# Kernel optimization log

Hardware: AMD Instinct MI355X
Metric: run time of the kernel (lower is better)

Reference implementation:

```python
import jax, jax.numpy as jnp
import numpy as np

A = 3                      # anchors per location
HS = [256, 128, 64, 32]    # square feature-map sizes (FPN levels)
B = 4                      # batch (num images)
SIZES = [A * h * h for h in HS]
T = sum(SIZES)             # 261120 anchors per image
PRE_N, POST_N = 512, 512
NMS_TH, SCORE_TH, MIN_SIZE = 0.7, 0.0, 1e-3
LOG_MAX = 4.135166556742356   # log(1000/16), standard delta clamp
MAXV = 8                      # max vertices of quad-quad intersection
LVL_OFF = 8192.0              # per-level coordinate offset for batched NMS


def box_corners(b):
    # b: [..., 5] (cx, cy, w, h, angle) -> [..., 4, 2] CCW corners
    cx, cy, w, h, a = (b[..., i] for i in range(5))
    c, s = jnp.cos(a), jnp.sin(a)
    dx = 0.5 * jnp.stack([w, -w, -w, w], -1)
    dy = 0.5 * jnp.stack([h, h, -h, -h], -1)
    x = cx[..., None] + dx * c[..., None] - dy * s[..., None]
    y = cy[..., None] + dx * s[..., None] + dy * c[..., None]
    return jnp.stack([x, y], -1)


def _clip(poly, cnt, p1, p2):
    # Sutherland-Hodgman clip of poly (padded [MAXV,2], cnt valid) by half-plane left of p1->p2
    e = p2 - p1
    d = e[0] * (poly[:, 1] - p1[1]) - e[1] * (poly[:, 0] - p1[0])
    def body(carry, i):
        out, oc = carry
        nxt = jnp.where(i + 1 < cnt, i + 1, 0)
        cur_in, nxt_in = d[i] >= 0, d[nxt] >= 0
        valid = i < cnt
        keep = valid & cur_in
        out = out.at[oc].set(jnp.where(keep, poly[i], out[oc]))
        oc = oc + keep.astype(jnp.int32)
        crs = valid & (cur_in != nxt_in)
        den = d[i] - d[nxt]
        t = d[i] / jnp.where(den == 0, 1.0, den)
        ip = poly[i] + t * (poly[nxt] - poly[i])
        out = out.at[oc].set(jnp.where(crs, ip, out[oc]))
        oc = oc + crs.astype(jnp.int32)
        return (out, oc), None
    (out, oc), _ = jax.lax.scan(body, (jnp.zeros((MAXV, 2), poly.dtype), jnp.int32(0)), jnp.arange(MAXV))
    return out, oc


def _inter_area(ca, cb):
    # intersection area of two convex quads given CCW corners [4,2]
    poly = jnp.zeros((MAXV, 2), ca.dtype).at[:4].set(ca)
    cnt = jnp.int32(4)
    for k in range(4):
        poly, cnt = _clip(poly, cnt, cb[k], cb[(k + 1) % 4])
    i = jnp.arange(MAXV)
    nxt = jnp.where(i + 1 < cnt, i + 1, 0)
    cr = poly[i, 0] * poly[nxt, 1] - poly[nxt, 0] * poly[i, 1]
    area = 0.5 * jnp.abs(jnp.sum(jnp.where(i < cnt, cr, 0.0)))
    return jnp.where(cnt >= 3, area, 0.0)


def decode(deltas, anchors):
    # XYWHA decode with 6-dim deltas (dx,dy,dw,dh,dsin,dcos), weights all 1.0
    ax, ay, aw, ah, aa = (anchors[..., i] for i in range(5))
    dx, dy, dw, dh, ds, dc = (deltas[..., i] for i in range(6))
    dw = jnp.minimum(dw, LOG_MAX)
    dh = jnp.minimum(dh, LOG_MAX)
    return jnp.stack([ax + dx * aw, ay + dy * ah, aw * jnp.exp(dw),
                      ah * jnp.exp(dh), aa + jnp.arctan2(ds, dc)], -1)


def nms_image(boxes, scores, levels):
    # boxes [N,5], scores [N] (post-sigmoid), levels [N] int32 -> fixed-size padded outputs
    N = scores.shape[0]
    valid = (boxes[:, 2] >= MIN_SIZE) & (boxes[:, 3] >= MIN_SIZE) & (scores >= SCORE_TH)
    s = jnp.where(valid, scores, -jnp.inf)
    order = jnp.argsort(-s)
    bx, sc, vd = boxes[order], s[order], valid[order]
    off = levels[order].astype(bx.dtype) * LVL_OFF
    nb = bx.at[:, :2].add(off[:, None])          # level offset => cross-level IoU == 0
    nbg = jax.lax.stop_gradient(nb)
    corners = box_corners(nbg)                    # [N,4,2]
    areas = nbg[:, 2] * nbg[:, 3]
    CH = 128
    def chunk_fn(args):
        cc, ca = args
        def row(ci, ai):
            inter = jax.vmap(lambda cj: _inter_area(ci, cj))(corners)
            return inter / (ai + areas - inter + 1e-7)
        return jax.vmap(row)(cc, ca)
    iou = jax.lax.map(chunk_fn, (corners.reshape(N // CH, CH, 4, 2),
                                 areas.reshape(N // CH, CH))).reshape(N, N)
    idx = jnp.arange(N)
    def body(i, sup):
        keep_i = ~sup[i]
        return sup | (keep_i & (iou[i] > NMS_TH) & (idx > i))
    sup = jax.lax.fori_loop(0, N, body, ~vd)      # invalid boxes start suppressed
    kept = ~sup
    _, top_i = jax.lax.top_k(jnp.where(kept, sc, -jnp.inf), POST_N)
    ok = kept[top_i]
    return jnp.where(ok[:, None], bx[top_i], 0.0), jnp.where(ok, sc[top_i], 0.0)


def rpn_forward(objs, dlts, anchors):
    obj_f, dlt_f = [], []
    for o, d, h in zip(objs, dlts, HS):
        # permute_and_flatten: [B,A,H,W] -> [B,H*W*A]; [B,A*6,H,W] -> [B,H*W*A,6]
        obj_f.append(o.transpose(0, 2, 3, 1).reshape(B, -1))
        dlt_f.append(d.reshape(B, A, 6, h, h).transpose(0, 3, 4, 1, 2).reshape(B, -1, 6))
    objectness = jnp.concatenate(obj_f, 1)        # [B, T]
    deltas = jnp.concatenate(dlt_f, 1)            # [B, T, 6]
    proposals = decode(deltas, anchors)           # [B, T, 5]
    parts, offset = [], 0
    for sz in SIZES:                               # per-level top-k
        k = min(PRE_N, sz)
        _, ti = jax.lax.top_k(objectness[:, offset:offset + sz], k)
        parts.append(ti + offset)
        offset += sz
    top_idx = jnp.concatenate(parts, 1)           # [B, 4*PRE_N]
    levels = jnp.concatenate([jnp.full((sz,), i, jnp.int32) for i, sz in enumerate(SIZES)])
    obj_top = jnp.take_along_axis(objectness, top_idx, 1)
    prop_top = jnp.take_along_axis(proposals, top_idx[..., None], 1)
    lvl_top = levels[top_idx]
    scores = jax.nn.sigmoid(obj_top)
    return jax.vmap(nms_image)(prop_top, scores, lvl_top)


def setup_inputs() -> dict:
    key = jax.random.key(0)
    ks = jax.random.split(key, 9)
    inp = {}
    for i, h in enumerate(HS):
        inp[f"obj{i}"] = jax.random.normal(ks[i], (B, A, h, h), jnp.float32)
        inp[f"dlt{i}"] = 0.25 * jax.random.normal(ks[4 + i], (B, A * 6, h, h), jnp.float32)
    u = jax.random.uniform(ks[8], (B, T, 5), jnp.float32)
    inp["anchors"] = jnp.stack([u[..., 0] * 1024.0, u[..., 1] * 1024.0,
                                8.0 + 120.0 * u[..., 2], 8.0 + 120.0 * u[..., 3],
                                jnp.pi * (u[..., 4] - 0.5)], -1)
    return inp


def reference(obj0, obj1, obj2, obj3, dlt0, dlt1, dlt2, dlt3, anchors):
    # returns (boxes [B, POST_N, 5], scores [B, POST_N]) padded with zeros
    return rpn_forward([obj0, obj1, obj2, obj3], [dlt0, dlt1, dlt2, dlt3], anchors)
```

## Files before the change

kernel.cpp:

```cpp
#include <hip/hip_runtime.h>

typedef unsigned int u32;
typedef unsigned long long u64;
typedef unsigned char u8;

#define NB 4
#define T_ANCH 261120
#define NCAND 2048
#define KSEL 512
#define POSTN 512
#define LOG_MAXF 4.135166556742356f
#define NMS_TH 0.7f
#define LVL_OFF_F 8192.0f
#define BINS 4096
#define EQCAP 8192
#define PAIR_CAP (1u<<20)
#define K4A_BLOCKS 2048
#define K4A_ROWS 4
#define K1_BLOCKS 256

__device__ __forceinline__ u32 mono32(float f){
  u32 u = __float_as_uint(f);
  return (u & 0x80000000u) ? ~u : (u | 0x80000000u);
}
__device__ __forceinline__ int lvl_hw(int lvl){ return 65536 >> (2*lvl); }
__device__ __forceinline__ int lvl_off(int lvl){
  return (lvl>0?196608:0) + (lvl>1?49152:0) + (lvl>2?12288:0);
}
__device__ __forceinline__ void k1_map(int bx, int& b, int& lvl, int& ch){
  b = bx >> 6;
  int c = bx & 63;
  if (c < 48){ lvl = 0; ch = c; }
  else if (c < 60){ lvl = 1; ch = c - 48; }
  else if (c < 63){ lvl = 2; ch = c - 60; }
  else { lvl = 3; ch = 0; }
}

__global__ __launch_bounds__(1024) void k1a_hist(
    const float* __restrict__ o0, const float* __restrict__ o1,
    const float* __restrict__ o2, const float* __restrict__ o3,
    u32* __restrict__ ghist)
{
  int b, lvl, ch;
  k1_map(blockIdx.x, b, lvl, ch);
  const float* ob = (lvl==0)?o0 : (lvl==1)?o1 : (lvl==2)?o2 : o3;
  int hw = lvl_hw(lvl);
  int size = 3*hw;
  int n4 = size >> 2;
  int i4 = ch*1024 + threadIdx.x;
  __shared__ u32 hist[BINS];
  for (int i = threadIdx.x; i < BINS; i += 1024) hist[i] = 0;
  __syncthreads();
  if (i4 < n4){
    float4 v = ((const float4*)(ob + (size_t)b*size))[i4];
    atomicAdd(&hist[mono32(v.x) >> 20], 1u);
    atomicAdd(&hist[mono32(v.y) >> 20], 1u);
    atomicAdd(&hist[mono32(v.z) >> 20], 1u);
    atomicAdd(&hist[mono32(v.w) >> 20], 1u);
  }
  __syncthreads();
  u32* out = ghist + (size_t)blockIdx.x*BINS;
  for (int i = threadIdx.x; i < BINS; i += 1024) out[i] = hist[i];
}

__global__ __launch_bounds__(1024) void k1b_thresh(
    const u32* __restrict__ ghist, u32* __restrict__ gb0,
    u32* __restrict__ gcA, u32* __restrict__ emitcnt, u32* __restrict__ tiecnt)
{
  int bid = blockIdx.x;
  int b = bid >> 2, lvl = bid & 3;
  int base_bx = b*64 + (lvl==0?0 : lvl==1?48 : lvl==2?60 : 63);
  int nch = (lvl==0?48 : lvl==1?12 : lvl==2?3 : 1);
  __shared__ u32 hist[BINS];
  __shared__ u32 coarse[64];
  int t = threadIdx.x;
  u32 c0=0,c1=0,c2=0,c3=0;
  for (int ch = 0; ch < nch; ++ch){
    const u32* h = ghist + (size_t)(base_bx+ch)*BINS;
    c0 += h[4*t+0]; c1 += h[4*t+1]; c2 += h[4*t+2]; c3 += h[4*t+3];
  }
  hist[4*t+0]=c0; hist[4*t+1]=c1; hist[4*t+2]=c2; hist[4*t+3]=c3;
  __syncthreads();
  if (t < 64){
    u32 s = 0;
    for (int z = 0; z < 64; ++z) s += hist[t*64 + z];
    coarse[t] = s;
  }
  __syncthreads();
  if (t == 0){
    u32 acc = 0;
    int cb = 63;
    while (acc + coarse[cb] < (u32)KSEL){ acc += coarse[cb]; --cb; }
    int z = cb*64 + 63;
    while (acc + hist[z] < (u32)KSEL){ acc += hist[z]; --z; }
    gb0[bid] = (u32)z;
    gcA[bid] = acc;
    emitcnt[bid] = 0;
    tiecnt[bid] = 0;
  }
}

__global__ __launch_bounds__(1024) void k1c_classify(
    const float* __restrict__ o0, const float* __restrict__ o1,
    const float* __restrict__ o2, const float* __restrict__ o3,
    const u32* __restrict__ gb0,
    u32* __restrict__ emitcnt, u32* __restrict__ tiecnt,
    int* __restrict__ cand_j, u64* __restrict__ gtie)
{
  int b, lvl, ch;
  k1_map(blockIdx.x, b, lvl, ch);
  int bid16 = b*4 + lvl;
  const float* ob = (lvl==0)?o0 : (lvl==1)?o1 : (lvl==2)?o2 : o3;
  int hw = lvl_hw(lvl);
  int size = 3*hw;
  int n4 = size >> 2;
  int i4 = ch*1024 + threadIdx.x;

  __shared__ u32 dbuf[KSEL];
  __shared__ u64 tbuf[4096];
  __shared__ u32 dn, tn, dbase, tbase;
  if (threadIdx.x == 0){ dn = 0; tn = 0; }
  __syncthreads();

  u32 b0v = gb0[bid16];
  if (i4 < n4){
    float4 v = ((const float4*)(ob + (size_t)b*size))[i4];
    int L = i4 << 2;
    int a = L / hw;
    int pix = L - a*hw;
    int j0 = pix*3 + a;
    float vv[4] = {v.x, v.y, v.z, v.w};
    #pragma unroll
    for (int q = 0; q < 4; ++q){
      u32 m = mono32(vv[q]);
      u32 bin = m >> 20;
      int j = j0 + 3*q;
      if (bin > b0v){
        u32 s = atomicAdd(&dn, 1u);
        if (s < (u32)KSEL) dbuf[s] = (u32)j;
      } else if (bin == b0v){
        u32 s = atomicAdd(&tn, 1u);
        if (s < 4096u) tbuf[s] = ((u64)m << 32) | (u32)(~(u32)j);
      }
    }
  }
  __syncthreads();
  if (threadIdx.x == 0){
    dbase = dn ? atomicAdd(&emitcnt[bid16], dn) : 0u;
    tbase = tn ? atomicAdd(&tiecnt[bid16], tn) : 0u;
  }
  __syncthreads();
  for (u32 x = threadIdx.x; x < dn; x += 1024){
    u32 s = dbase + x;
    if (s < (u32)KSEL) cand_j[bid16*KSEL + s] = (int)dbuf[x];
  }
  for (u32 x = threadIdx.x; x < tn; x += 1024){
    u32 s = tbase + x;
    if (s < (u32)EQCAP) gtie[(size_t)bid16*EQCAP + s] = tbuf[x];
  }
}

__global__ __launch_bounds__(1024) void k1d_tie(
    const u64* __restrict__ gtie, const u32* __restrict__ tiecnt,
    const u32* __restrict__ gcA, u32* __restrict__ emitcnt,
    int* __restrict__ cand_j)
{
  int bid = blockIdx.x;
  __shared__ u64 eq[EQCAP];
  __shared__ u32 wbuf[KSEL];
  __shared__ u32 wn, wbase;
  u32 n = tiecnt[bid]; if (n > (u32)EQCAP) n = (u32)EQCAP;
  u32 k = (u32)KSEL - gcA[bid];
  if (threadIdx.x == 0) wn = 0;
  for (u32 i = threadIdx.x; i < n; i += 1024) eq[i] = gtie[(size_t)bid*EQCAP + i];
  __syncthreads();
  for (u32 i = threadIdx.x; i < n; i += 1024){
    u64 ki = eq[i];
    u32 r = 0;
    for (u32 m = 0; m < n; ++m) r += (eq[m] > ki) ? 1u : 0u;
    if (r < k){
      u32 s = atomicAdd(&wn, 1u);
      if (s < (u32)KSEL) wbuf[s] = (u32)(~(u32)ki);
    }
  }
  __syncthreads();
  if (threadIdx.x == 0) wbase = wn ? atomicAdd(&emitcnt[bid], wn) : 0u;
  __syncthreads();
  for (u32 x = threadIdx.x; x < wn; x += 1024){
    u32 s = wbase + x;
    if (s < (u32)KSEL) cand_j[bid*KSEL + s] = (int)wbuf[x];
  }
}

__global__ __launch_bounds__(256) void k2_decode(
    const float* __restrict__ o0, const float* __restrict__ o1,
    const float* __restrict__ o2, const float* __restrict__ o3,
    const float* __restrict__ d0, const float* __restrict__ d1,
    const float* __restrict__ d2, const float* __restrict__ d3,
    const float* __restrict__ anchors,
    const int* __restrict__ cand_j,
    float* __restrict__ cscore, u32* __restrict__ csmono,
    u64* __restrict__ ctb, float* __restrict__ cbox, u8* __restrict__ cvalid)
{
  int c = blockIdx.x*256 + threadIdx.x;
  if (c >= NB*NCAND) return;
  int pair = c >> 9;
  int b = pair >> 2, lvl = pair & 3;
  int j = cand_j[c];
  int hw = lvl_hw(lvl);
  u32 pix = (u32)j / 3u;
  u32 a = (u32)j - pix*3u;
  const float* ob = (lvl==0)?o0 : (lvl==1)?o1 : (lvl==2)?o2 : o3;
  const float* dl = (lvl==0)?d0 : (lvl==1)?d1 : (lvl==2)?d2 : d3;

  float ov = ob[(size_t)(b*3 + (int)a)*hw + pix];
  size_t dbase = ((size_t)(b*3 + (int)a)*6)*(size_t)hw + pix;
  float dx  = dl[dbase + 0*(size_t)hw];
  float dy  = dl[dbase + 1*(size_t)hw];
  float dw  = dl[dbase + 2*(size_t)hw];
  float dh  = dl[dbase + 3*(size_t)hw];
  float dsn = dl[dbase + 4*(size_t)hw];
  float dcs = dl[dbase + 5*(size_t)hw];
  int tt = lvl_off(lvl) + j;
  const float* an = anchors + ((size_t)b*T_ANCH + tt)*5;
  float ax=an[0], ay=an[1], aw=an[2], ah=an[3], aa=an[4];
  dw = fminf(dw, LOG_MAXF); dh = fminf(dh, LOG_MAXF);
  float cx = ax + dx*aw;
  float cy = ay + dy*ah;
  float w  = aw * expf(dw);
  float h  = ah * expf(dh);
  float ang = aa + atan2f(dsn, dcs);
  double sd = 1.0 / (1.0 + exp(-(double)ov));
  float sc = (float)sd;
  bool valid = (w >= 1e-3f) && (h >= 1e-3f) && (sc >= 0.0f);
  cscore[c] = sc;
  csmono[c] = valid ? mono32(sc) : 0u;
  ctb[c] = ((u64)lvl << 50) | ((u64)(u32)(~mono32(ov)) << 18) | (u64)(u32)j;
  cvalid[c] = valid ? 1 : 0;
  float* bb = cbox + (size_t)c*5;
  bb[0]=cx; bb[1]=cy; bb[2]=w; bb[3]=h; bb[4]=ang;
}

__global__ __launch_bounds__(256) void k3_rank(
    const u32* __restrict__ csmono, const u64* __restrict__ ctb,
    const float* __restrict__ cscore, const float* __restrict__ cbox,
    const u8* __restrict__ cvalid,
    float* __restrict__ sscore, float* __restrict__ sbox,
    float* __restrict__ geom, float4* __restrict__ aabb4,
    u8* __restrict__ svalid)
{
  int b   = blockIdx.x >> 6;
  int blk = blockIdx.x & 63;
  __shared__ u32 sm[NCAND];
  __shared__ u64 stb[NCAND];
  __shared__ u32 cnt[32][8];
  for (int k = threadIdx.x; k < NCAND; k += 256){
    sm[k]  = csmono[b*NCAND + k];
    stb[k] = ctb[b*NCAND + k];
  }
  __syncthreads();
  int esub = threadIdx.x >> 3;
  int ssub = threadIdx.x & 7;
  int id = blk*32 + esub;
  u32 ms = sm[id];
  u64 mt = stb[id];
  u32 r = 0;
  #pragma unroll 8
  for (int it = 0; it < 256; ++it){
    int m = it*8 + ssub;
    u32 s2 = sm[m]; u64 t2 = stb[m];
    r += ((s2 > ms) || (s2 == ms && t2 < mt)) ? 1u : 0u;
  }
  cnt[esub][ssub] = r;
  __syncthreads();
  if (ssub == 0){
    u32 rank = 0;
    #pragma unroll
    for (int q = 0; q < 8; ++q) rank += cnt[esub][q];
    int gsrc = b*NCAND + id;
    int gdst = b*NCAND + (int)rank;
    sscore[gdst] = cscore[gsrc];
    svalid[gdst] = cvalid[gsrc];
    float b0 = cbox[(size_t)gsrc*5+0], b1 = cbox[(size_t)gsrc*5+1];
    float b2 = cbox[(size_t)gsrc*5+2], b3 = cbox[(size_t)gsrc*5+3];
    float b4 = cbox[(size_t)gsrc*5+4];
    float* sb = sbox + (size_t)gdst*5;
    sb[0]=b0; sb[1]=b1; sb[2]=b2; sb[3]=b3; sb[4]=b4;
    int lvl = (int)((mt >> 50) & 3ull);
    float offv = (float)lvl * LVL_OFF_F;
    float cx = b0 + offv, cy = b1 + offv, w=b2, h=b3, ang=b4;
    float cc = cosf(ang), sn = sinf(ang);
    float hx = 0.5f*w, hy = 0.5f*h;
    float x0 = cx + hx*cc - hy*sn, y0 = cy + hx*sn + hy*cc;
    float x1 = cx - hx*cc - hy*sn, y1 = cy - hx*sn + hy*cc;
    float x2 = cx - hx*cc + hy*sn, y2 = cy - hx*sn - hy*cc;
    float x3 = cx + hx*cc + hy*sn, y3 = cy + hx*sn - hy*cc;
    float minx = fminf(fminf(x0,x1),fminf(x2,x3));
    float maxx = fmaxf(fmaxf(x0,x1),fmaxf(x2,x3));
    float miny = fminf(fminf(y0,y1),fminf(y2,y3));
    float maxy = fmaxf(fmaxf(y0,y1),fmaxf(y2,y3));
    float* g = geom + (size_t)gdst*16;
    g[0]=minx; g[1]=maxx; g[2]=miny; g[3]=maxy; g[4]=w*h;
    g[5]=x0; g[6]=y0; g[7]=x1; g[8]=y1; g[9]=x2; g[10]=y2; g[11]=x3; g[12]=y3;
    aabb4[gdst] = make_float4(minx, maxx, miny, maxy);
  }
}

__global__ __launch_bounds__(256) void k4a_aabb(
    const float4* __restrict__ aabb4,
    u32* __restrict__ list, u32* __restrict__ gcount)
{
  __shared__ u32 lbuf[K4A_ROWS*NCAND];
  __shared__ u32 lcnt, lbase;
  if (threadIdx.x == 0) lcnt = 0;
  __syncthreads();
  int img = blockIdx.x >> 9;
  int i0  = (blockIdx.x & 511) * K4A_ROWS;
  #pragma unroll
  for (int r = 0; r < K4A_ROWS; ++r){
    int i = i0 + r;
    float4 gi = aabb4[img*NCAND + i];
    for (int j = threadIdx.x; j < NCAND; j += 256){
      bool pass = false;
      if (j > i){
        float4 gj = aabb4[img*NCAND + j];
        pass = !(gi.x > gj.y || gj.x > gi.y || gi.z > gj.w || gj.z > gi.w);
      }
      if (pass){
        u32 s = atomicAdd(&lcnt, 1u);
        lbuf[s] = (u32)((img << 22) | (i << 11) | j);
      }
    }
  }
  __syncthreads();
  if (threadIdx.x == 0) lbase = lcnt ? atomicAdd(gcount, lcnt) : 0u;
  __syncthreads();
  u32 n = lcnt, bs = lbase;
  for (u32 x = threadIdx.x; x < n; x += 256){
    u32 idx = bs + x;
    if (idx < PAIR_CAP) list[idx] = lbuf[x];
  }
}

__device__ __forceinline__ void emit_pt(float* ox, float* oy, int oc, float x, float y){
  #pragma unroll
  for (int s = 0; s < 8; ++s) if (s == oc){ ox[s] = x; oy[s] = y; }
}

__device__ float quad_inter(const float* ca, const float* cb){
  float px[8], py[8];
  #pragma unroll
  for (int q = 0; q < 8; ++q){ px[q]=0.f; py[q]=0.f; }
  #pragma unroll
  for (int q = 0; q < 4; ++q){ px[q]=ca[2*q]; py[q]=ca[2*q+1]; }
  int cnt = 4;
  #pragma unroll
  for (int e = 0; e < 4; ++e){
    float p1x = cb[2*e],         p1y = cb[2*e+1];
    float p2x = cb[(2*e+2)&7],   p2y = cb[(2*e+3)&7];
    float ex = p2x-p1x, ey = p2y-p1y;
    float d[8];
    #pragma unroll
    for (int q = 0; q < 8; ++q) d[q] = ex*(py[q]-p1y) - ey*(px[q]-p1x);
    float ox[8], oy[8];
    #pragma unroll
    for (int q = 0; q < 8; ++q){ ox[q]=0.f; oy[q]=0.f; }
    int oc = 0;
    #pragma unroll
    for (int q = 0; q < 8; ++q){
      if (q < cnt){
        bool last = (q+1 >= cnt);
        float dn  = last ? d[0]  : d[(q+1)&7];
        bool in0 = (d[q] >= 0.0f), in1 = (dn >= 0.0f);
        if (in0){ emit_pt(ox,oy,oc,px[q],py[q]); oc++; }
        if (in0 != in1){
          float pnx = last ? px[0] : px[(q+1)&7];
          float pny = last ? py[0] : py[(q+1)&7];
          float den = d[q] - dn;
          float t = d[q] / ((den == 0.0f) ? 1.0f : den);
          emit_pt(ox,oy,oc, px[q] + t*(pnx-px[q]), py[q] + t*(pny-py[q]));
          oc++;
        }
      }
    }
    cnt = (oc > 8) ? 8 : oc;
    #pragma unroll
    for (int q = 0; q < 8; ++q){ px[q]=ox[q]; py[q]=oy[q]; }
  }
  if (cnt < 3) return 0.0f;
  float s = 0.0f;
  #pragma unroll
  for (int q = 0; q < 8; ++q){
    if (q < cnt){
      bool last = (q+1 >= cnt);
      float pnx = last ? px[0] : px[(q+1)&7];
      float pny = last ? py[0] : py[(q+1)&7];
      s += px[q]*pny - pnx*py[q];
    }
  }
  return 0.5f*fabsf(s);
}

__global__ __launch_bounds__(256) void k4b_clip(
    const float* __restrict__ geom, const u32* __restrict__ list,
    const u32* __restrict__ gcount, u64* __restrict__ mask,
    u64* __restrict__ rowflag)
{
  u32 count = *gcount;
  if (count > PAIR_CAP) count = PAIR_CAP;
  for (u32 idx = blockIdx.x*256 + threadIdx.x; idx < count; idx += gridDim.x*256){
    u32 gt = list[idx];
    int img = (int)(gt >> 22);
    int rem = (int)(gt & ((1u<<22)-1));
    int i = rem >> 11;
    int j = rem & (NCAND-1);
    const float* gi = geom + ((size_t)(img*NCAND + i))*16;
    const float* gj = geom + ((size_t)(img*NCAND + j))*16;
    float inter = quad_inter(gi+5, gj+5);
    float iou = inter / (gi[4] + gj[4] - inter + 1e-7f);
    if (iou > NMS_TH){
      atomicOr(&mask[((size_t)(img*NCAND + i))*32 + (j >> 6)], 1ull << (j & 63));
      atomicOr(&rowflag[(size_t)img*32 + (i >> 6)], 1ull << (i & 63));
    }
  }
}

__global__ __launch_bounds__(1024) void k5_nms_out(
    const u64* __restrict__ mask, const u64* __restrict__ rowflag,
    const u8* __restrict__ svalid,
    const float* __restrict__ sbox, const float* __restrict__ sscore,
    float* __restrict__ out)
{
  int b = blockIdx.x;
  __shared__ u32 fid[NCAND];
  __shared__ u32 wcnt[32], wpref[32];
  __shared__ u64 s_kept[32];
  __shared__ u32 pref[32];
  __shared__ u32 s_F;
  int t = threadIdx.x;
  int wid = t >> 6, lane = t & 63;

  if (t < 32) wcnt[t] = (u32)__popcll(rowflag[b*32 + t]);
  __syncthreads();
  if (t == 0){
    u32 run = 0;
    for (int w = 0; w < 32; ++w){ wpref[w] = run; run += wcnt[w]; }
    s_F = run;
  }
  __syncthreads();
  if (t < 32){
    u64 fw = rowflag[b*32 + t];
    u32 o = wpref[t];
    while (fw){
      int bpos = __builtin_ctzll(fw);
      fid[o++] = (u32)(t*64 + bpos);
      fw &= fw - 1;
    }
  }
  for (int x = t; x < POSTN*5; x += 1024) out[(size_t)b*POSTN*5 + x] = 0.0f;
  for (int x = t; x < POSTN;   x += 1024) out[(size_t)NB*POSTN*5 + b*POSTN + x] = 0.0f;
  __syncthreads();

  if (wid == 0){
    u32 slo = 0, shi = 0;
    {
      int wl = lane & 31;
      u64 w = 0;
      for (int q = 0; q < 64; ++q)
        if (!svalid[b*NCAND + wl*64 + q]) w |= (1ull << q);
      slo = (u32)w; shi = (u32)(w >> 32);
    }
    u32 F = s_F;
    const u64* mb = mask + ((size_t)b*NCAND)*32;
    for (u32 f = 0; f < F; f += 8){
      u32 myfid = 0;
      if (f + (lane & 7) < F) myfid = fid[f + (lane & 7)];
      u64 v[8];
      #pragma unroll
      for (int q = 0; q < 8; ++q){
        if (f + q < F){
          u32 fq = (u32)__builtin_amdgcn_readlane((int)myfid, q);
          v[q] = mb[(size_t)fq*32 + (lane & 31)];
        } else v[q] = 0ull;
      }
      #pragma unroll
      for (int q = 0; q < 8; ++q){
        if (f + q < F){
          u32 i = (u32)__builtin_amdgcn_readlane((int)myfid, q);
          int wi = (int)(i >> 6);
          u32 wlo = (u32)__builtin_amdgcn_readlane((int)slo, wi);
          u32 whi = (u32)__builtin_amdgcn_readlane((int)shi, wi);
          u64 w = ((u64)whi << 32) | wlo;
          u32 keep = (u32)((~w >> (i & 63)) & 1ull);
          u64 vm = v[q] & (0ull - (u64)keep);
          slo |= (u32)vm; shi |= (u32)(vm >> 32);
        }
      }
    }
    if (lane < 32) s_kept[lane] = ~(((u64)shi << 32) | slo);
  }
  __syncthreads();

  if (t < 32) pref[t] = (u32)__popcll(s_kept[t]);
  __syncthreads();
  if (t == 0){
    u32 run = 0;
    for (int w = 0; w < 32; ++w){ u32 tv = pref[w]; pref[w] = run; run += tv; }
  }
  __syncthreads();
  for (int i = t; i < NCAND; i += 1024){
    u64 kw = s_kept[i >> 6];
    if ((kw >> (i & 63)) & 1ull){
      u32 rank = pref[i >> 6] + (u32)__popcll(kw & ((1ull << (i & 63)) - 1ull));
      if (rank < POSTN){
        const float* bp = sbox + ((size_t)(b*NCAND + i))*5;
        float* op = out + ((size_t)(b*POSTN + rank))*5;
        op[0]=bp[0]; op[1]=bp[1]; op[2]=bp[2]; op[3]=bp[3]; op[4]=bp[4];
        out[(size_t)NB*POSTN*5 + b*POSTN + rank] = sscore[b*NCAND + i];
      }
    }
  }
}

extern "C" void kernel_launch(void* const* d_in, const int* in_sizes, int n_in,
                              void* d_out, int out_size, void* d_ws, size_t ws_size,
                              hipStream_t stream)
{
  (void)out_size; (void)ws_size;
  const float *obj[4] = {nullptr,nullptr,nullptr,nullptr};
  const float *dlt[4] = {nullptr,nullptr,nullptr,nullptr};
  const float *anchors = nullptr;
  for (int i = 0; i < n_in; ++i){
    int s = in_sizes[i];
    const float* p = (const float*)d_in[i];
    switch (s){
      case 786432:  obj[0] = p; break;
      case 4718592: dlt[0] = p; break;
      case 196608:  obj[1] = p; break;
      case 1179648: dlt[1] = p; break;
      case 49152:   obj[2] = p; break;
      case 294912:  dlt[2] = p; break;
      case 12288:   obj[3] = p; break;
      case 73728:   dlt[3] = p; break;
      case 5222400: anchors = p; break;
      default: break;
    }
  }

  char* wsb = (char*)d_ws;
  size_t off = 0;
  auto alloc = [&](size_t bytes)->void*{
    size_t cur = (off + 255) & ~(size_t)255;
    off = cur + bytes;
    return (void*)(wsb + cur);
  };
  int*   cand_j = (int*)  alloc(16*KSEL*sizeof(int));
  float* cscore = (float*)alloc((size_t)NB*NCAND*sizeof(float));
  u32*   csmono = (u32*)  alloc((size_t)NB*NCAND*sizeof(u32));
  u64*   ctb    = (u64*)  alloc((size_t)NB*NCAND*sizeof(u64));
  float* cbox   = (float*)alloc((size_t)NB*NCAND*5*sizeof(float));
  u8*    cvalid = (u8*)   alloc((size_t)NB*NCAND);
  float* sscore = (float*)alloc((size_t)NB*NCAND*sizeof(float));
  float* sbox   = (float*)alloc((size_t)NB*NCAND*5*sizeof(float));
  u8*    svalid = (u8*)   alloc((size_t)NB*NCAND);
  float* geom   = (float*)alloc((size_t)NB*NCAND*16*sizeof(float));
  float4* aabb4 = (float4*)alloc((size_t)NB*NCAND*sizeof(float4));
  size_t mask_bytes = (size_t)NB*NCAND*32*sizeof(u64);
  u64*   maskp  = (u64*)  alloc(mask_bytes);
  u64*   rowflag= (u64*)  alloc((size_t)NB*32*sizeof(u64));
  u32*   pcount = (u32*)  alloc(sizeof(u32));
  u32*   plist  = (u32*)  alloc((size_t)PAIR_CAP*sizeof(u32));
  u32*   ghist  = (u32*)  alloc((size_t)K1_BLOCKS*BINS*sizeof(u32));
  u64*   gtie   = (u64*)  alloc((size_t)16*EQCAP*sizeof(u64));
  u32*   gb0    = (u32*)  alloc(16*sizeof(u32));
  u32*   gcA    = (u32*)  alloc(16*sizeof(u32));
  u32*   emitc  = (u32*)  alloc(16*sizeof(u32));
  u32*   tiec   = (u32*)  alloc(16*sizeof(u32));

  hipMemsetAsync(maskp, 0, mask_bytes + (size_t)NB*32*sizeof(u64) + 256, stream);

  hipLaunchKernelGGL(k1a_hist, dim3(K1_BLOCKS), dim3(1024), 0, stream,
                     obj[0], obj[1], obj[2], obj[3], ghist);
  hipLaunchKernelGGL(k1b_thresh, dim3(16), dim3(1024), 0, stream,
                     ghist, gb0, gcA, emitc, tiec);
  hipLaunchKernelGGL(k1c_classify, dim3(K1_BLOCKS), dim3(1024), 0, stream,
                     obj[0], obj[1], obj[2], obj[3], gb0, emitc, tiec,
                     cand_j, gtie);
  hipLaunchKernelGGL(k1d_tie, dim3(16), dim3(1024), 0, stream,
                     gtie, tiec, gcA, emitc, cand_j);
  hipLaunchKernelGGL(k2_decode, dim3(32), dim3(256), 0, stream,
                     obj[0], obj[1], obj[2], obj[3],
                     dlt[0], dlt[1], dlt[2], dlt[3],
                     anchors, cand_j, cscore, csmono, ctb, cbox, cvalid);
  hipLaunchKernelGGL(k3_rank, dim3(256), dim3(256), 0, stream,
                     csmono, ctb, cscore, cbox, cvalid, sscore, sbox, geom,
                     aabb4, svalid);
  hipLaunchKernelGGL(k4a_aabb, dim3(K4A_BLOCKS), dim3(256), 0, stream,
                     aabb4, plist, pcount);
  hipLaunchKernelGGL(k4b_clip, dim3(256), dim3(256), 0, stream,
                     geom, plist, pcount, maskp, rowflag);
  hipLaunchKernelGGL(k5_nms_out, dim3(4), dim3(1024), 0, stream,
                     maskp, rowflag, svalid, sbox, sscore, (float*)d_out);
}
```

Baseline: 200.5 us.

## Fuse pipeline stages to cut kernel launches and global round-trips

Merges the histogram and threshold kernels using global atomic histograms and a last-block-done counter, so the final block per (image, level) computes the threshold. Tie resolution is fused with box decode, and the AABB pair filter is fused with the quad clipping, which removes the global pair list. The aim is to cut launch count and intermediate global traffic. In exchange, clipping load is now spread unevenly across blocks, and extra atomics and fences are added.

```diff
diff --git a/kernel.cpp b/kernel.cpp
--- a/kernel.cpp
+++ b/kernel.cpp
@@ -14,7 +14,6 @@
 #define LVL_OFF_F 8192.0f
 #define BINS 4096
 #define EQCAP 8192
-#define PAIR_CAP (1u<<20)
 #define K4A_BLOCKS 2048
 #define K4A_ROWS 4
 #define K1_BLOCKS 256
@@ -36,19 +35,24 @@
   else { lvl = 3; ch = 0; }
 }
 
-__global__ __launch_bounds__(1024) void k1a_hist(
+__global__ __launch_bounds__(1024) void k1_hist_thresh(
     const float* __restrict__ o0, const float* __restrict__ o1,
     const float* __restrict__ o2, const float* __restrict__ o3,
-    u32* __restrict__ ghist)
+    u32* __restrict__ hist16, u32* __restrict__ done16,
+    u32* __restrict__ gb0, u32* __restrict__ gcA)
 {
   int b, lvl, ch;
   k1_map(blockIdx.x, b, lvl, ch);
+  int bid16 = b*4 + lvl;
+  int nch = (lvl==0?48 : lvl==1?12 : lvl==2?3 : 1);
   const float* ob = (lvl==0)?o0 : (lvl==1)?o1 : (lvl==2)?o2 : o3;
   int hw = lvl_hw(lvl);
   int size = 3*hw;
   int n4 = size >> 2;
   int i4 = ch*1024 + threadIdx.x;
   __shared__ u32 hist[BINS];
+  __shared__ u32 coarse[64];
+  __shared__ int s_last;
   for (int i = threadIdx.x; i < BINS; i += 1024) hist[i] = 0;
   __syncthreads();
   if (i4 < n4){
@@ -59,28 +63,25 @@
     atomicAdd(&hist[mono32(v.w) >> 20], 1u);
   }
   __syncthreads();
-  u32* out = ghist + (size_t)blockIdx.x*BINS;
-  for (int i = threadIdx.x; i < BINS; i += 1024) out[i] = hist[i];
-}
-
-__global__ __launch_bounds__(1024) void k1b_thresh(
-    const u32* __restrict__ ghist, u32* __restrict__ gb0,
-    u32* __restrict__ gcA, u32* __restrict__ emitcnt, u32* __restrict__ tiecnt)
-{
-  int bid = blockIdx.x;
-  int b = bid >> 2, lvl = bid & 3;
-  int base_bx = b*64 + (lvl==0?0 : lvl==1?48 : lvl==2?60 : 63);
-  int nch = (lvl==0?48 : lvl==1?12 : lvl==2?3 : 1);
-  __shared__ u32 hist[BINS];
-  __shared__ u32 coarse[64];
+  u32* gh = hist16 + (size_t)bid16*BINS;
+  for (int i = threadIdx.x; i < BINS; i += 1024){
+    u32 c = hist[i];
+    if (c) atomicAdd(&gh[i], c);
+  }
+  __syncthreads();
+  if (threadIdx.x == 0){
+    __threadfence();
+    u32 d = atomicAdd(&done16[bid16], 1u);
+    s_last = (d == (u32)(nch - 1)) ? 1 : 0;
+  }
+  __syncthreads();
+  if (!s_last) return;
+
+  __threadfence();
+  for (int i = threadIdx.x; i < BINS; i += 1024)
+    hist[i] = __hip_atomic_load(&gh[i], __ATOMIC_RELAXED, __HIP_MEMORY_SCOPE_AGENT);
+  __syncthreads();
   int t = threadIdx.x;
-  u32 c0=0,c1=0,c2=0,c3=0;
-  for (int ch = 0; ch < nch; ++ch){
-    const u32* h = ghist + (size_t)(base_bx+ch)*BINS;
-    c0 += h[4*t+0]; c1 += h[4*t+1]; c2 += h[4*t+2]; c3 += h[4*t+3];
-  }
-  hist[4*t+0]=c0; hist[4*t+1]=c1; hist[4*t+2]=c2; hist[4*t+3]=c3;
-  __syncthreads();
   if (t < 64){
     u32 s = 0;
     for (int z = 0; z < 64; ++z) s += hist[t*64 + z];
@@ -93,14 +94,12 @@
     while (acc + coarse[cb] < (u32)KSEL){ acc += coarse[cb]; --cb; }
     int z = cb*64 + 63;
     while (acc + hist[z] < (u32)KSEL){ acc += hist[z]; --z; }
-    gb0[bid] = (u32)z;
-    gcA[bid] = acc;
-    emitcnt[bid] = 0;
-    tiecnt[bid] = 0;
-  }
-}
-
-__global__ __launch_bounds__(1024) void k1c_classify(
+    gb0[bid16] = (u32)z;
+    gcA[bid16] = acc;
+  }
+}
+
+__global__ __launch_bounds__(1024) void k2_classify(
     const float* __restrict__ o0, const float* __restrict__ o1,
     const float* __restrict__ o2, const float* __restrict__ o3,
     const u32* __restrict__ gb0,
@@ -160,21 +159,31 @@
   }
 }
 
-__global__ __launch_bounds__(1024) void k1d_tie(
+__global__ __launch_bounds__(512) void k3_tie_decode(
     const u64* __restrict__ gtie, const u32* __restrict__ tiecnt,
-    const u32* __restrict__ gcA, u32* __restrict__ emitcnt,
-    int* __restrict__ cand_j)
+    const u32* __restrict__ gcA, const int* __restrict__ cand_j,
+    const float* __restrict__ o0, const float* __restrict__ o1,
+    const float* __restrict__ o2, const float* __restrict__ o3,
+    const float* __restrict__ d0, const float* __restrict__ d1,
+    const float* __restrict__ d2, const float* __restrict__ d3,
+    const float* __restrict__ anchors,
+    float* __restrict__ cscore, u32* __restrict__ csmono,
+    u64* __restrict__ ctb, float* __restrict__ cbox, u8* __restrict__ cvalid)
 {
   int bid = blockIdx.x;
+  int t = threadIdx.x;
   __shared__ u64 eq[EQCAP];
   __shared__ u32 wbuf[KSEL];
-  __shared__ u32 wn, wbase;
+  __shared__ int jlist[KSEL];
+  __shared__ u32 wn;
   u32 n = tiecnt[bid]; if (n > (u32)EQCAP) n = (u32)EQCAP;
-  u32 k = (u32)KSEL - gcA[bid];
-  if (threadIdx.x == 0) wn = 0;
-  for (u32 i = threadIdx.x; i < n; i += 1024) eq[i] = gtie[(size_t)bid*EQCAP + i];
-  __syncthreads();
-  for (u32 i = threadIdx.x; i < n; i += 1024){
+  u32 cA = gcA[bid];
+  u32 k = (u32)KSEL - cA;
+  if (t == 0) wn = 0;
+  for (int i = t; i < KSEL; i += 512) jlist[i] = 0;
+  for (u32 i = t; i < n; i += 512) eq[i] = gtie[(size_t)bid*EQCAP + i];
+  __syncthreads();
+  for (u32 i = t; i < n; i += 512){
     u64 ki = eq[i];
     u32 r = 0;
     for (u32 m = 0; m < n; ++m) r += (eq[m] > ki) ? 1u : 0u;
@@ -184,64 +193,55 @@
     }
   }
   __syncthreads();
-  if (threadIdx.x == 0) wbase = wn ? atomicAdd(&emitcnt[bid], wn) : 0u;
-  __syncthreads();
-  for (u32 x = threadIdx.x; x < wn; x += 1024){
-    u32 s = wbase + x;
-    if (s < (u32)KSEL) cand_j[bid*KSEL + s] = (int)wbuf[x];
-  }
-}
-
-__global__ __launch_bounds__(256) void k2_decode(
-    const float* __restrict__ o0, const float* __restrict__ o1,
-    const float* __restrict__ o2, const float* __restrict__ o3,
-    const float* __restrict__ d0, const float* __restrict__ d1,
-    const float* __restrict__ d2, const float* __restrict__ d3,
-    const float* __restrict__ anchors,
-    const int* __restrict__ cand_j,
-    float* __restrict__ cscore, u32* __restrict__ csmono,
-    u64* __restrict__ ctb, float* __restrict__ cbox, u8* __restrict__ cvalid)
-{
-  int c = blockIdx.x*256 + threadIdx.x;
-  if (c >= NB*NCAND) return;
-  int pair = c >> 9;
-  int b = pair >> 2, lvl = pair & 3;
-  int j = cand_j[c];
-  int hw = lvl_hw(lvl);
-  u32 pix = (u32)j / 3u;
-  u32 a = (u32)j - pix*3u;
-  const float* ob = (lvl==0)?o0 : (lvl==1)?o1 : (lvl==2)?o2 : o3;
-  const float* dl = (lvl==0)?d0 : (lvl==1)?d1 : (lvl==2)?d2 : d3;
-
-  float ov = ob[(size_t)(b*3 + (int)a)*hw + pix];
-  size_t dbase = ((size_t)(b*3 + (int)a)*6)*(size_t)hw + pix;
-  float dx  = dl[dbase + 0*(size_t)hw];
-  float dy  = dl[dbase + 1*(size_t)hw];
-  float dw  = dl[dbase + 2*(size_t)hw];
-  float dh  = dl[dbase + 3*(size_t)hw];
-  float dsn = dl[dbase + 4*(size_t)hw];
-  float dcs = dl[dbase + 5*(size_t)hw];
-  int tt = lvl_off(lvl) + j;
-  const float* an = anchors + ((size_t)b*T_ANCH + tt)*5;
-  float ax=an[0], ay=an[1], aw=an[2], ah=an[3], aa=an[4];
-  dw = fminf(dw, LOG_MAXF); dh = fminf(dh, LOG_MAXF);
-  float cx = ax + dx*aw;
-  float cy = ay + dy*ah;
-  float w  = aw * expf(dw);
-  float h  = ah * expf(dh);
-  float ang = aa + atan2f(dsn, dcs);
-  double sd = 1.0 / (1.0 + exp(-(double)ov));
-  float sc = (float)sd;
-  bool valid = (w >= 1e-3f) && (h >= 1e-3f) && (sc >= 0.0f);
-  cscore[c] = sc;
-  csmono[c] = valid ? mono32(sc) : 0u;
-  ctb[c] = ((u64)lvl << 50) | ((u64)(u32)(~mono32(ov)) << 18) | (u64)(u32)j;
-  cvalid[c] = valid ? 1 : 0;
-  float* bb = cbox + (size_t)c*5;
-  bb[0]=cx; bb[1]=cy; bb[2]=w; bb[3]=h; bb[4]=ang;
-}
-
-__global__ __launch_bounds__(256) void k3_rank(
+  u32 w = wn;
+  for (u32 i = t; i < cA; i += 512)
+    if (i < (u32)KSEL) jlist[i] = cand_j[bid*KSEL + i];
+  for (u32 x = t; x < w; x += 512){
+    u32 s = cA + x;
+    if (s < (u32)KSEL) jlist[s] = (int)wbuf[x];
+  }
+  __syncthreads();
+
+  {
+    int c = bid*KSEL + t;
+    int b = bid >> 2, lvl = bid & 3;
+    int j = jlist[t];
+    int hw = lvl_hw(lvl);
+    u32 pix = (u32)j / 3u;
+    u32 a = (u32)j - pix*3u;
+    const float* ob = (lvl==0)?o0 : (lvl==1)?o1 : (lvl==2)?o2 : o3;
+    const float* dl = (lvl==0)?d0 : (lvl==1)?d1 : (lvl==2)?d2 : d3;
+
+    float ov = ob[(size_t)(b*3 + (int)a)*hw + pix];
+    size_t dbase = ((size_t)(b*3 + (int)a)*6)*(size_t)hw + pix;
+    float dx  = dl[dbase + 0*(size_t)hw];
+    float dy  = dl[dbase + 1*(size_t)hw];
+    float dw  = dl[dbase + 2*(size_t)hw];
+    float dh  = dl[dbase + 3*(size_t)hw];
+    float dsn = dl[dbase + 4*(size_t)hw];
+    float dcs = dl[dbase + 5*(size_t)hw];
+    int tt = lvl_off(lvl) + j;
+    const float* an = anchors + ((size_t)b*T_ANCH + tt)*5;
+    float ax=an[0], ay=an[1], aw=an[2], ah=an[3], aa=an[4];
+    dw = fminf(dw, LOG_MAXF); dh = fminf(dh, LOG_MAXF);
+    float cx = ax + dx*aw;
+    float cy = ay + dy*ah;
+    float ww = aw * expf(dw);
+    float hh = ah * expf(dh);
+    float ang = aa + atan2f(dsn, dcs);
+    double sd = 1.0 / (1.0 + exp(-(double)ov));
+    float sc = (float)sd;
+    bool valid = (ww >= 1e-3f) && (hh >= 1e-3f) && (sc >= 0.0f);
+    cscore[c] = sc;
+    csmono[c] = valid ? mono32(sc) : 0u;
+    ctb[c] = ((u64)lvl << 50) | ((u64)(u32)(~mono32(ov)) << 18) | (u64)(u32)j;
+    cvalid[c] = valid ? 1 : 0;
+    float* bb = cbox + (size_t)c*5;
+    bb[0]=cx; bb[1]=cy; bb[2]=ww; bb[3]=hh; bb[4]=ang;
+  }
+}
+
+__global__ __launch_bounds__(256) void k4_rank(
     const u32* __restrict__ csmono, const u64* __restrict__ ctb,
     const float* __restrict__ cscore, const float* __restrict__ cbox,
     const u8* __restrict__ cvalid,
@@ -303,42 +303,6 @@
     g[0]=minx; g[1]=maxx; g[2]=miny; g[3]=maxy; g[4]=w*h;
     g[5]=x0; g[6]=y0; g[7]=x1; g[8]=y1; g[9]=x2; g[10]=y2; g[11]=x3; g[12]=y3;
     aabb4[gdst] = make_float4(minx, maxx, miny, maxy);
-  }
-}
-
-__global__ __launch_bounds__(256) void k4a_aabb(
-    const float4* __restrict__ aabb4,
-    u32* __restrict__ list, u32* __restrict__ gcount)
-{
-  __shared__ u32 lbuf[K4A_ROWS*NCAND];
-  __shared__ u32 lcnt, lbase;
-  if (threadIdx.x == 0) lcnt = 0;
-  __syncthreads();
-  int img = blockIdx.x >> 9;
-  int i0  = (blockIdx.x & 511) * K4A_ROWS;
-  #pragma unroll
-  for (int r = 0; r < K4A_ROWS; ++r){
-    int i = i0 + r;
-    float4 gi = aabb4[img*NCAND + i];
-    for (int j = threadIdx.x; j < NCAND; j += 256){
-      bool pass = false;
-      if (j > i){
-        float4 gj = aabb4[img*NCAND + j];
-        pass = !(gi.x > gj.y || gj.x > gi.y || gi.z > gj.w || gj.z > gi.w);
-      }
-      if (pass){
-        u32 s = atomicAdd(&lcnt, 1u);
-        lbuf[s] = (u32)((img << 22) | (i << 11) | j);
-      }
-    }
-  }
-  __syncthreads();
-  if (threadIdx.x == 0) lbase = lcnt ? atomicAdd(gcount, lcnt) : 0u;
-  __syncthreads();
-  u32 n = lcnt, bs = lbase;
-  for (u32 x = threadIdx.x; x < n; x += 256){
-    u32 idx = bs + x;
-    if (idx < PAIR_CAP) list[idx] = lbuf[x];
   }
 }
 
@@ -401,19 +365,38 @@
   return 0.5f*fabsf(s);
 }
 
-__global__ __launch_bounds__(256) void k4b_clip(
-    const float* __restrict__ geom, const u32* __restrict__ list,
-    const u32* __restrict__ gcount, u64* __restrict__ mask,
-    u64* __restrict__ rowflag)
-{
-  u32 count = *gcount;
-  if (count > PAIR_CAP) count = PAIR_CAP;
-  for (u32 idx = blockIdx.x*256 + threadIdx.x; idx < count; idx += gridDim.x*256){
-    u32 gt = list[idx];
-    int img = (int)(gt >> 22);
-    int rem = (int)(gt & ((1u<<22)-1));
-    int i = rem >> 11;
-    int j = rem & (NCAND-1);
+__global__ __launch_bounds__(256) void k5_pairs(
+    const float4* __restrict__ aabb4, const float* __restrict__ geom,
+    u64* __restrict__ mask, u64* __restrict__ rowflag)
+{
+  __shared__ u32 lbuf[K4A_ROWS*NCAND];
+  __shared__ u32 lcnt;
+  if (threadIdx.x == 0) lcnt = 0;
+  __syncthreads();
+  int img = blockIdx.x >> 9;
+  int i0  = (blockIdx.x & 511) * K4A_ROWS;
+  #pragma unroll
+  for (int r = 0; r < K4A_ROWS; ++r){
+    int i = i0 + r;
+    float4 gi = aabb4[img*NCAND + i];
+    for (int j = threadIdx.x; j < NCAND; j += 256){
+      bool pass = false;
+      if (j > i){
+        float4 gj = aabb4[img*NCAND + j];
+        pass = !(gi.x > gj.y || gj.x > gi.y || gi.z > gj.w || gj.z > gi.w);
+      }
+      if (pass){
+        u32 s = atomicAdd(&lcnt, 1u);
+        lbuf[s] = (u32)((i << 11) | j);
+      }
+    }
+  }
+  __syncthreads();
+  u32 n = lcnt;
+  for (u32 x = threadIdx.x; x < n; x += 256){
+    u32 gt = lbuf[x];
+    int i = (int)(gt >> 11);
+    int j = (int)(gt & (NCAND-1));
     const float* gi = geom + ((size_t)(img*NCAND + i))*16;
     const float* gj = geom + ((size_t)(img*NCAND + j))*16;
     float inter = quad_inter(gi+5, gj+5);
@@ -425,7 +408,7 @@
   }
 }
 
-__global__ __launch_bounds__(1024) void k5_nms_out(
+__global__ __launch_bounds__(1024) void k6_nms_out(
     const u64* __restrict__ mask, const u64* __restrict__ rowflag,
     const u8* __restrict__ svalid,
     const float* __restrict__ sbox, const float* __restrict__ sscore,
@@ -565,40 +548,35 @@
   u8*    svalid = (u8*)   alloc((size_t)NB*NCAND);
   float* geom   = (float*)alloc((size_t)NB*NCAND*16*sizeof(float));
   float4* aabb4 = (float4*)alloc((size_t)NB*NCAND*sizeof(float4));
+  u64*   gtie   = (u64*)  alloc((size_t)16*EQCAP*sizeof(u64));
+  u32*   gb0    = (u32*)  alloc(16*sizeof(u32));
+  u32*   gcA    = (u32*)  alloc(16*sizeof(u32));
   size_t mask_bytes = (size_t)NB*NCAND*32*sizeof(u64);
   u64*   maskp  = (u64*)  alloc(mask_bytes);
   u64*   rowflag= (u64*)  alloc((size_t)NB*32*sizeof(u64));
-  u32*   pcount = (u32*)  alloc(sizeof(u32));
-  u32*   plist  = (u32*)  alloc((size_t)PAIR_CAP*sizeof(u32));
-  u32*   ghist  = (u32*)  alloc((size_t)K1_BLOCKS*BINS*sizeof(u32));
-  u64*   gtie   = (u64*)  alloc((size_t)16*EQCAP*sizeof(u64));
-  u32*   gb0    = (u32*)  alloc(16*sizeof(u32));
-  u32*   gcA    = (u32*)  alloc(16*sizeof(u32));
+  u32*   hist16 = (u32*)  alloc((size_t)16*BINS*sizeof(u32));
+  u32*   done16 = (u32*)  alloc(16*sizeof(u32));
   u32*   emitc  = (u32*)  alloc(16*sizeof(u32));
   u32*   tiec   = (u32*)  alloc(16*sizeof(u32));
-
-  hipMemsetAsync(maskp, 0, mask_bytes + (size_t)NB*32*sizeof(u64) + 256, stream);
-
-  hipLaunchKernelGGL(k1a_hist, dim3(K1_BLOCKS), dim3(1024), 0, stream,
-                     obj[0], obj[1], obj[2], obj[3], ghist);
-  hipLaunchKernelGGL(k1b_thresh, dim3(16), dim3(1024), 0, stream,
-                     ghist, gb0, gcA, emitc, tiec);
-  hipLaunchKernelGGL(k1c_classify, dim3(K1_BLOCKS), dim3(1024), 0, stream,
+  size_t zero_len = (size_t)((wsb + off) - (char*)maskp);
+
+  hipMemsetAsync(maskp, 0, zero_len, stream);
+
+  hipLaunchKernelGGL(k1_hist_thresh, dim3(K1_BLOCKS), dim3(1024), 0, stream,
+                     obj[0], obj[1], obj[2], obj[3], hist16, done16, gb0, gcA);
+  hipLaunchKernelGGL(k2_classify, dim3(K1_BLOCKS), dim3(1024), 0, stream,
                      obj[0], obj[1], obj[2], obj[3], gb0, emitc, tiec,
                      cand_j, gtie);
-  hipLaunchKernelGGL(k1d_tie, dim3(16), dim3(1024), 0, stream,
-                     gtie, tiec, gcA, emitc, cand_j);
-  hipLaunchKernelGGL(k2_decode, dim3(32), dim3(256), 0, stream,
+  hipLaunchKernelGGL(k3_tie_decode, dim3(16), dim3(512), 0, stream,
+                     gtie, tiec, gcA, cand_j,
                      obj[0], obj[1], obj[2], obj[3],
                      dlt[0], dlt[1], dlt[2], dlt[3],
-                     anchors, cand_j, cscore, csmono, ctb, cbox, cvalid);
-  hipLaunchKernelGGL(k3_rank, dim3(256), dim3(256), 0, stream,
+                     anchors, cscore, csmono, ctb, cbox, cvalid);
+  hipLaunchKernelGGL(k4_rank, dim3(256), dim3(256), 0, stream,
                      csmono, ctb, cscore, cbox, cvalid, sscore, sbox, geom,
                      aabb4, svalid);
-  hipLaunchKernelGGL(k4a_aabb, dim3(K4A_BLOCKS), dim3(256), 0, stream,
-                     aabb4, plist, pcount);
-  hipLaunchKernelGGL(k4b_clip, dim3(256), dim3(256), 0, stream,
-                     geom, plist, pcount, maskp, rowflag);
-  hipLaunchKernelGGL(k5_nms_out, dim3(4), dim3(1024), 0, stream,
+  hipLaunchKernelGGL(k5_pairs, dim3(K4A_BLOCKS), dim3(256), 0, stream,
+                     aabb4, geom, maskp, rowflag);
+  hipLaunchKernelGGL(k6_nms_out, dim3(4), dim3(1024), 0, stream,
                      maskp, rowflag, svalid, sbox, sscore, (float*)d_out);
 }
```

New measurement: 204.6 us. 2.1% more time.
